# Kernel tuning notes

Hardware: AMD Instinct MI355X
Metric: run time of the kernel (lower is better)

## Reference

```python
import jax, jax.numpy as jnp
import numpy as np

N_NODES = 100000
N_EDGES = 3200000
D_IN = 256
D_OUT = 128
LN_EPS = 1e-5


def setup_inputs() -> dict:
    key = jax.random.key(0)
    ks = jax.random.split(key, 6)
    stdv = 1.0 / np.sqrt(D_OUT)
    x = jax.random.normal(ks[0], (N_NODES, D_IN), dtype=jnp.float32)
    weight = jax.random.uniform(ks[1], (D_IN, D_OUT), minval=-stdv, maxval=stdv, dtype=jnp.float32)
    bias = jnp.zeros((D_OUT,), dtype=jnp.float32)
    res_w = jax.random.normal(ks[2], (D_IN, D_OUT), dtype=jnp.float32) * 0.05
    res_b = jnp.zeros((D_OUT,), dtype=jnp.float32)
    ln_gamma = jnp.ones((D_OUT,), dtype=jnp.float32)
    ln_beta = jnp.zeros((D_OUT,), dtype=jnp.float32)
    edge_weight = jax.random.uniform(ks[3], (N_EDGES,), dtype=jnp.float32)
    edge_index = jax.random.randint(ks[4], (2, N_EDGES), 0, N_NODES, dtype=jnp.int32)
    return {"x": x, "weight": weight, "bias": bias, "res_w": res_w, "res_b": res_b,
            "ln_gamma": ln_gamma, "ln_beta": ln_beta,
            "edge_weight": edge_weight, "edge_index": edge_index}


def reference(x, weight, bias, res_w, res_b, ln_gamma, ln_beta, edge_weight, edge_index):
    # dense projection: [N, D_IN] @ [D_IN, D_OUT]
    support = x @ weight
    # spmm: out[dst] += w_e * support[src]  (weighted COO aggregation)
    src, dst = edge_index[0], edge_index[1]
    msg = support[src] * edge_weight[:, None]          # [E, D_OUT]
    out = jax.ops.segment_sum(msg, dst, num_segments=N_NODES)
    # fused bias + activated residual branch
    out = out + bias + jax.nn.relu(x @ res_w + res_b)
    # layernorm over feature dim
    mu = jnp.mean(out, axis=-1, keepdims=True)
    var = jnp.mean(jnp.square(out - mu), axis=-1, keepdims=True)
    out = (out - mu) * jax.lax.rsqrt(var + LN_EPS) * ln_gamma + ln_beta
    return out
```

## Files before the change

kernel.cpp:

```cpp
#include <hip/hip_runtime.h>
#include <hip/hip_bf16.h>

#define D_IN 256
#define D_OUT 128
#define LN_EPS 1e-5f
#define NBUCK 256
#define NCHUNK 256

typedef short bf16x8 __attribute__((ext_vector_type(8)));
typedef float f32x4 __attribute__((ext_vector_type(4)));
typedef unsigned short ushort_t;

__device__ __forceinline__ float b2f(ushort_t u) {
    union { unsigned int i; float f; } v; v.i = (unsigned int)u << 16; return v.f;
}
__device__ __forceinline__ ushort_t f2b(float f) {
    __hip_bfloat16 h = __float2bfloat16(f);
    return *reinterpret_cast<ushort_t*>(&h);
}

__global__ void k_transpose(const float* __restrict__ w, const float* __restrict__ rw,
                            ushort_t* __restrict__ wt) {
    int idx = blockIdx.x * 256 + threadIdx.x;
    int n = idx >> 8, k = idx & 255;
    float v = (n < 128) ? w[k * 128 + n] : rw[k * 128 + (n - 128)];
    wt[idx] = f2b(v);
}

__launch_bounds__(256)
__global__ void k_gemm(const float* __restrict__ x, const ushort_t* __restrict__ wt,
                       const float* __restrict__ bias, const float* __restrict__ res_b,
                       ushort_t* __restrict__ support, float* __restrict__ out, int n_nodes) {
    __shared__ ushort_t As[64 * 40];
    __shared__ ushort_t Bs[256 * 40];

    const int tid = threadIdx.x;
    const int m0 = blockIdx.x * 64;
    const int wv = tid >> 6, lane = tid & 63;
    const int lm = lane & 15, quad = lane >> 4;
    const int mh = wv >> 1;
    const int nh = wv & 1;

    f32x4 acc[2][8];
#pragma unroll
    for (int i = 0; i < 2; i++)
#pragma unroll
        for (int j = 0; j < 8; j++) acc[i][j] = 0.0f;

    const int arow = tid >> 2, aseg = tid & 3;
    const bool arow_ok = (m0 + arow) < n_nodes;
    const float* xrow = x + (long)(m0 + arow) * D_IN + aseg * 8;

    for (int kc = 0; kc < 8; kc++) {
        __syncthreads();
        {
            bf16x8 av = {0, 0, 0, 0, 0, 0, 0, 0};
            if (arow_ok) {
                f32x4 p0 = *(const f32x4*)(xrow + kc * 32);
                f32x4 p1 = *(const f32x4*)(xrow + kc * 32 + 4);
#pragma unroll
                for (int j = 0; j < 4; j++) { av[j] = (short)f2b(p0[j]); av[4 + j] = (short)f2b(p1[j]); }
            }
            *(bf16x8*)(&As[arow * 40 + aseg * 8]) = av;
        }
#pragma unroll
        for (int i = 0; i < 4; i++) {
            int n = (tid >> 2) + i * 64;
            bf16x8 v = *(const bf16x8*)(wt + n * 256 + kc * 32 + aseg * 8);
            *(bf16x8*)(&Bs[n * 40 + aseg * 8]) = v;
        }
        __syncthreads();

        bf16x8 afr0 = *(const bf16x8*)(&As[(mh * 32 + lm) * 40 + quad * 8]);
        bf16x8 afr1 = *(const bf16x8*)(&As[(mh * 32 + 16 + lm) * 40 + quad * 8]);
#pragma unroll
        for (int nt = 0; nt < 8; nt++) {
            bf16x8 bfr = *(const bf16x8*)(&Bs[(nh * 128 + nt * 16 + lm) * 40 + quad * 8]);
            acc[0][nt] = __builtin_amdgcn_mfma_f32_16x16x32_bf16(afr0, bfr, acc[0][nt], 0, 0, 0);
            acc[1][nt] = __builtin_amdgcn_mfma_f32_16x16x32_bf16(afr1, bfr, acc[1][nt], 0, 0, 0);
        }
    }

#pragma unroll
    for (int i = 0; i < 2; i++) {
#pragma unroll
        for (int nt = 0; nt < 8; nt++) {
            int col = nh * 128 + nt * 16 + lm;
#pragma unroll
            for (int r = 0; r < 4; r++) {
                int node = m0 + mh * 32 + i * 16 + quad * 4 + r;
                if (node >= n_nodes) continue;
                float v = acc[i][nt][r];
                if (col < 128) {
                    support[(long)node * 128 + col] = f2b(v);
                } else {
                    int c2 = col - 128;
                    float t = v + res_b[c2];
                    t = t > 0.0f ? t : 0.0f;
                    out[(long)node * 128 + c2] = t + bias[c2];
                }
            }
        }
    }
}

__launch_bounds__(256)
__global__ void k_count(const int* __restrict__ ei, int* __restrict__ cntmat, int E, int chunk) {
    __shared__ int h[NBUCK];
    int c = blockIdx.x, t = threadIdx.x;
    h[t] = 0;
    __syncthreads();
    int lo = c * chunk, hi = min(lo + chunk, E);
    for (int e = lo + t; e < hi; e += 256)
        atomicAdd(&h[(unsigned)ei[E + e] >> 9], 1);
    __syncthreads();
    cntmat[t * NCHUNK + c] = h[t];
}

__launch_bounds__(256)
__global__ void k_scan1(int* __restrict__ cntmat, int* __restrict__ rowsum) {
    __shared__ int sh[256];
    int b = blockIdx.x, t = threadIdx.x;
    int v = cntmat[b * NCHUNK + t];
    sh[t] = v;
    __syncthreads();
    for (int off = 1; off < 256; off <<= 1) {
        int x = sh[t]; int add = (t >= off) ? sh[t - off] : 0;
        __syncthreads(); sh[t] = x + add; __syncthreads();
    }
    cntmat[b * NCHUNK + t] = sh[t] - v;
    if (t == 255) rowsum[b] = sh[255];
}

__launch_bounds__(256)
__global__ void k_scan2(const int* __restrict__ rowsum, int* __restrict__ bucket_base,
                        int* __restrict__ offs, int n_nodes, int E) {
    __shared__ int sh[256];
    int t = threadIdx.x;
    int v = rowsum[t];
    sh[t] = v;
    __syncthreads();
    for (int off = 1; off < 256; off <<= 1) {
        int x = sh[t]; int add = (t >= off) ? sh[t - off] : 0;
        __syncthreads(); sh[t] = x + add; __syncthreads();
    }
    bucket_base[t] = sh[t] - v;
    if (t == 255) bucket_base[256] = sh[255];
    if (t == 0) offs[n_nodes] = E;
}

__launch_bounds__(256)
__global__ void k_part(const int* __restrict__ ei, const float* __restrict__ ew,
                       const int* __restrict__ cntmat, const int* __restrict__ bucket_base,
                       int* __restrict__ pk, ushort_t* __restrict__ pw, int E, int chunk) {
    __shared__ int cur[NBUCK];
    int c = blockIdx.x, t = threadIdx.x;
    cur[t] = bucket_base[t] + cntmat[t * NCHUNK + c];
    __syncthreads();
    int lo = c * chunk, hi = min(lo + chunk, E);
    for (int e = lo + t; e < hi; e += 256) {
        int src = ei[e];
        int dst = ei[E + e];
        float w = ew[e];
        int b = (unsigned)dst >> 9;
        int pos = atomicAdd(&cur[b], 1);
        pk[pos] = src | ((dst & 511) << 17);
        pw[pos] = f2b(w);
    }
}

__launch_bounds__(256)
__global__ void k_build(const int* __restrict__ pk, const ushort_t* __restrict__ pw,
                        const int* __restrict__ bucket_base, int* __restrict__ sk,
                        ushort_t* __restrict__ sw, int* __restrict__ offs, int n_nodes) {
    __shared__ int h[512];
    __shared__ int psum[256];
    int b = blockIdx.x, t = threadIdx.x;
    int start = bucket_base[b], end = bucket_base[b + 1];
    h[t] = 0; h[t + 256] = 0;
    __syncthreads();
    for (int i = start + t; i < end; i += 256)
        atomicAdd(&h[(unsigned)pk[i] >> 17], 1);
    __syncthreads();
    int h0 = h[2 * t], h1 = h[2 * t + 1];
    int p = h0 + h1;
    psum[t] = p;
    __syncthreads();
    for (int off = 1; off < 256; off <<= 1) {
        int x = psum[t]; int add = (t >= off) ? psum[t - off] : 0;
        __syncthreads(); psum[t] = x + add; __syncthreads();
    }
    int e0 = psum[t] - p;
    int e1 = e0 + h0;
    h[2 * t] = e0; h[2 * t + 1] = e1;
    int node0 = b * 512 + 2 * t;
    if (node0 < n_nodes) offs[node0] = start + e0;
    if (node0 + 1 < n_nodes) offs[node0 + 1] = start + e1;
    __syncthreads();
    for (int i = start + t; i < end; i += 256) {
        int key = pk[i];
        int dl = (unsigned)key >> 17;
        int pos = start + atomicAdd(&h[dl], 1);
        sk[pos] = key;
        sw[pos] = pw[i];
    }
}

__launch_bounds__(256)
__global__ void k_agg_ln(const ushort_t* __restrict__ support, const int* __restrict__ offs,
                         const int* __restrict__ sk, const ushort_t* __restrict__ sw,
                         const float* __restrict__ gamma, const float* __restrict__ beta,
                         float* __restrict__ out, int n_nodes) {
    int gw = (int)((blockIdx.x * blockDim.x + threadIdx.x) >> 6);
    int lane = threadIdx.x & 63;
    int nw = (int)((gridDim.x * blockDim.x) >> 6);
    float g0 = gamma[lane * 2], g1 = gamma[lane * 2 + 1];
    float b0 = beta[lane * 2], b1 = beta[lane * 2 + 1];

    for (int node = gw; node < n_nodes; node += nw) {
        int start = offs[node], end = offs[node + 1];
        float ax = 0.0f, ay = 0.0f;
        for (int base = start; base < end; base += 64) {
            int n = end - base; if (n > 64) n = 64;
            int key = 0, wbits = 0;
            if (lane < n) {
                key = sk[base + lane];
                wbits = (int)sw[base + lane];
            }
            int j = 0;
            for (; j + 4 <= n; j += 4) {
                int s0 = __builtin_amdgcn_readlane(key, j + 0) & 131071;
                int s1 = __builtin_amdgcn_readlane(key, j + 1) & 131071;
                int s2 = __builtin_amdgcn_readlane(key, j + 2) & 131071;
                int s3 = __builtin_amdgcn_readlane(key, j + 3) & 131071;
                float w0 = b2f((ushort_t)__builtin_amdgcn_readlane(wbits, j + 0));
                float w1 = b2f((ushort_t)__builtin_amdgcn_readlane(wbits, j + 1));
                float w2 = b2f((ushort_t)__builtin_amdgcn_readlane(wbits, j + 2));
                float w3 = b2f((ushort_t)__builtin_amdgcn_readlane(wbits, j + 3));
                unsigned int v0 = *(const unsigned int*)(support + (long)s0 * 128 + lane * 2);
                unsigned int v1 = *(const unsigned int*)(support + (long)s1 * 128 + lane * 2);
                unsigned int v2 = *(const unsigned int*)(support + (long)s2 * 128 + lane * 2);
                unsigned int v3 = *(const unsigned int*)(support + (long)s3 * 128 + lane * 2);
                ax += w0 * b2f((ushort_t)(v0 & 0xffffu)) + w1 * b2f((ushort_t)(v1 & 0xffffu))
                    + w2 * b2f((ushort_t)(v2 & 0xffffu)) + w3 * b2f((ushort_t)(v3 & 0xffffu));
                ay += w0 * b2f((ushort_t)(v0 >> 16)) + w1 * b2f((ushort_t)(v1 >> 16))
                    + w2 * b2f((ushort_t)(v2 >> 16)) + w3 * b2f((ushort_t)(v3 >> 16));
            }
            for (; j < n; j++) {
                int sj = __builtin_amdgcn_readlane(key, j) & 131071;
                float wj = b2f((ushort_t)__builtin_amdgcn_readlane(wbits, j));
                unsigned int v = *(const unsigned int*)(support + (long)sj * 128 + lane * 2);
                ax += wj * b2f((ushort_t)(v & 0xffffu));
                ay += wj * b2f((ushort_t)(v >> 16));
            }
        }
        float2 r = *(const float2*)(out + (long)node * 128 + lane * 2);
        float tx = ax + r.x, ty = ay + r.y;
        float s = tx + ty;
        float ss = tx * tx + ty * ty;
#pragma unroll
        for (int off = 1; off < 64; off <<= 1) {
            s += __shfl_xor(s, off, 64);
            ss += __shfl_xor(ss, off, 64);
        }
        float mean = s * (1.0f / 128.0f);
        float var = ss * (1.0f / 128.0f) - mean * mean;
        float rstd = rsqrtf(var + LN_EPS);
        float2 o;
        o.x = (tx - mean) * rstd * g0 + b0;
        o.y = (ty - mean) * rstd * g1 + b1;
        *(float2*)(out + (long)node * 128 + lane * 2) = o;
    }
}

extern "C" void kernel_launch(void* const* d_in, const int* in_sizes, int n_in,
                              void* d_out, int out_size, void* d_ws, size_t ws_size,
                              hipStream_t stream) {
    const float* x      = (const float*)d_in[0];
    const float* weight = (const float*)d_in[1];
    const float* bias   = (const float*)d_in[2];
    const float* res_w  = (const float*)d_in[3];
    const float* res_b  = (const float*)d_in[4];
    const float* gamma  = (const float*)d_in[5];
    const float* beta   = (const float*)d_in[6];
    const float* ew     = (const float*)d_in[7];
    const int*   ei     = (const int*)d_in[8];

    const int E = in_sizes[7];
    const int n_nodes = in_sizes[0] / D_IN;
    const int chunk = (E + NCHUNK - 1) / NCHUNK;
    float* out = (float*)d_out;

    char* ws = (char*)d_ws;
    size_t off = 0;
    auto alloc = [&](size_t bytes) { void* p = ws + off; off = (off + bytes + 255) & ~(size_t)255; return p; };
    ushort_t* wt      = (ushort_t*)alloc(256 * 256 * 2);
    ushort_t* support = (ushort_t*)alloc((size_t)n_nodes * 128 * 2);
    int* cntmat       = (int*)alloc((size_t)NBUCK * NCHUNK * 4);
    int* rowsum       = (int*)alloc(NBUCK * 4);
    int* bucket_base  = (int*)alloc((NBUCK + 1) * 4);
    int* offs         = (int*)alloc((size_t)(n_nodes + 1) * 4);
    int* pk           = (int*)alloc((size_t)E * 4);
    ushort_t* pw      = (ushort_t*)alloc((size_t)E * 2);
    int* sk           = (int*)alloc((size_t)E * 4);
    ushort_t* sw      = (ushort_t*)alloc((size_t)E * 2);

    k_transpose<<<256, 256, 0, stream>>>(weight, res_w, wt);
    k_gemm<<<(n_nodes + 63) / 64, 256, 0, stream>>>(x, wt, bias, res_b, support, out, n_nodes);
    k_count<<<NCHUNK, 256, 0, stream>>>(ei, cntmat, E, chunk);
    k_scan1<<<NBUCK, 256, 0, stream>>>(cntmat, rowsum);
    k_scan2<<<1, 256, 0, stream>>>(rowsum, bucket_base, offs, n_nodes, E);
    k_part<<<NCHUNK, 256, 0, stream>>>(ei, ew, cntmat, bucket_base, pk, pw, E, chunk);
    k_build<<<NBUCK, 256, 0, stream>>>(pk, pw, bucket_base, sk, sw, offs, n_nodes);
    k_agg_ln<<<4096, 256, 0, stream>>>(support, offs, sk, sw, gamma, beta, out, n_nodes);
}
```

Measured before the change: 505.1 us.

## Use finer dst buckets and half-wave edge-pair gathers in aggregation

The bucket sort now uses 256 nodes per bucket (about 391 buckets) with 512 edge chunks and ushort counts, so the partition and build passes get more parallel blocks with smaller local histograms. k_build runs 512 threads per block and writes the source index pre-masked. In the aggregation each half-wave handles one edge of a pair and loads 4 bf16 per lane, halving the loop trips, then the halves are combined with a shuffle. The change also overlaps the count matrix with the transposed-weight buffer to save workspace, which relies on the weight buffer no longer being needed after the GEMM. It also assumes per-chunk bucket counts fit in 16 bits and that nbuck is at most 512.

```diff
diff --git a/kernel.cpp b/kernel.cpp
--- a/kernel.cpp
+++ b/kernel.cpp
@@ -4,8 +4,8 @@
 #define D_IN 256
 #define D_OUT 128
 #define LN_EPS 1e-5f
-#define NBUCK 256
-#define NCHUNK 256
+#define NPB 256
+#define NCHUNK 512
 
 typedef short bf16x8 __attribute__((ext_vector_type(8)));
 typedef float f32x4 __attribute__((ext_vector_type(4)));
@@ -105,103 +105,112 @@
 }
 
 __launch_bounds__(256)
-__global__ void k_count(const int* __restrict__ ei, int* __restrict__ cntmat, int E, int chunk) {
-    __shared__ int h[NBUCK];
+__global__ void k_count(const int* __restrict__ ei, ushort_t* __restrict__ cntmat,
+                        int E, int chunk, int nbuck) {
+    __shared__ int h[512];
     int c = blockIdx.x, t = threadIdx.x;
-    h[t] = 0;
+    h[t] = 0; h[t + 256] = 0;
     __syncthreads();
     int lo = c * chunk, hi = min(lo + chunk, E);
     for (int e = lo + t; e < hi; e += 256)
-        atomicAdd(&h[(unsigned)ei[E + e] >> 9], 1);
-    __syncthreads();
-    cntmat[t * NCHUNK + c] = h[t];
-}
-
-__launch_bounds__(256)
-__global__ void k_scan1(int* __restrict__ cntmat, int* __restrict__ rowsum) {
+        atomicAdd(&h[(unsigned)ei[E + e] >> 8], 1);
+    __syncthreads();
+    for (int i = t; i < nbuck; i += 256)
+        cntmat[i * NCHUNK + c] = (ushort_t)h[i];
+}
+
+__launch_bounds__(256)
+__global__ void k_scan1(ushort_t* __restrict__ cntmat, int* __restrict__ rowsum) {
     __shared__ int sh[256];
     int b = blockIdx.x, t = threadIdx.x;
-    int v = cntmat[b * NCHUNK + t];
-    sh[t] = v;
+    int v0 = cntmat[b * NCHUNK + 2 * t];
+    int v1 = cntmat[b * NCHUNK + 2 * t + 1];
+    int s = v0 + v1;
+    sh[t] = s;
     __syncthreads();
     for (int off = 1; off < 256; off <<= 1) {
         int x = sh[t]; int add = (t >= off) ? sh[t - off] : 0;
         __syncthreads(); sh[t] = x + add; __syncthreads();
     }
-    cntmat[b * NCHUNK + t] = sh[t] - v;
+    int e = sh[t] - s;
+    cntmat[b * NCHUNK + 2 * t] = (ushort_t)e;
+    cntmat[b * NCHUNK + 2 * t + 1] = (ushort_t)(e + v0);
     if (t == 255) rowsum[b] = sh[255];
 }
 
-__launch_bounds__(256)
+__launch_bounds__(512)
 __global__ void k_scan2(const int* __restrict__ rowsum, int* __restrict__ bucket_base,
-                        int* __restrict__ offs, int n_nodes, int E) {
-    __shared__ int sh[256];
+                        int* __restrict__ offs, int n_nodes, int E, int nbuck) {
+    __shared__ int sh[512];
     int t = threadIdx.x;
-    int v = rowsum[t];
+    int v = (t < nbuck) ? rowsum[t] : 0;
     sh[t] = v;
     __syncthreads();
-    for (int off = 1; off < 256; off <<= 1) {
+    for (int off = 1; off < 512; off <<= 1) {
         int x = sh[t]; int add = (t >= off) ? sh[t - off] : 0;
         __syncthreads(); sh[t] = x + add; __syncthreads();
     }
-    bucket_base[t] = sh[t] - v;
-    if (t == 255) bucket_base[256] = sh[255];
+    if (t < nbuck) bucket_base[t] = sh[t] - v;
+    if (t == nbuck - 1) bucket_base[nbuck] = sh[t];
     if (t == 0) offs[n_nodes] = E;
 }
 
 __launch_bounds__(256)
 __global__ void k_part(const int* __restrict__ ei, const float* __restrict__ ew,
-                       const int* __restrict__ cntmat, const int* __restrict__ bucket_base,
-                       int* __restrict__ pk, ushort_t* __restrict__ pw, int E, int chunk) {
-    __shared__ int cur[NBUCK];
+                       const ushort_t* __restrict__ cntmat, const int* __restrict__ bucket_base,
+                       int* __restrict__ pk, ushort_t* __restrict__ pw, int E, int chunk, int nbuck) {
+    __shared__ int cur[512];
     int c = blockIdx.x, t = threadIdx.x;
-    cur[t] = bucket_base[t] + cntmat[t * NCHUNK + c];
+    for (int i = t; i < nbuck; i += 256)
+        cur[i] = bucket_base[i] + (int)cntmat[i * NCHUNK + c];
     __syncthreads();
     int lo = c * chunk, hi = min(lo + chunk, E);
     for (int e = lo + t; e < hi; e += 256) {
         int src = ei[e];
         int dst = ei[E + e];
         float w = ew[e];
-        int b = (unsigned)dst >> 9;
+        int b = (unsigned)dst >> 8;
         int pos = atomicAdd(&cur[b], 1);
-        pk[pos] = src | ((dst & 511) << 17);
+        pk[pos] = src | ((dst & 255) << 17);
         pw[pos] = f2b(w);
     }
 }
 
-__launch_bounds__(256)
+__launch_bounds__(512)
 __global__ void k_build(const int* __restrict__ pk, const ushort_t* __restrict__ pw,
                         const int* __restrict__ bucket_base, int* __restrict__ sk,
                         ushort_t* __restrict__ sw, int* __restrict__ offs, int n_nodes) {
-    __shared__ int h[512];
+    __shared__ int h[256];
     __shared__ int psum[256];
     int b = blockIdx.x, t = threadIdx.x;
     int start = bucket_base[b], end = bucket_base[b + 1];
-    h[t] = 0; h[t + 256] = 0;
-    __syncthreads();
-    for (int i = start + t; i < end; i += 256)
+    if (t < 256) h[t] = 0;
+    __syncthreads();
+    for (int i = start + t; i < end; i += 512)
         atomicAdd(&h[(unsigned)pk[i] >> 17], 1);
     __syncthreads();
-    int h0 = h[2 * t], h1 = h[2 * t + 1];
-    int p = h0 + h1;
-    psum[t] = p;
+    int cnt = 0;
+    if (t < 256) { cnt = h[t]; psum[t] = cnt; }
     __syncthreads();
     for (int off = 1; off < 256; off <<= 1) {
-        int x = psum[t]; int add = (t >= off) ? psum[t - off] : 0;
-        __syncthreads(); psum[t] = x + add; __syncthreads();
-    }
-    int e0 = psum[t] - p;
-    int e1 = e0 + h0;
-    h[2 * t] = e0; h[2 * t + 1] = e1;
-    int node0 = b * 512 + 2 * t;
-    if (node0 < n_nodes) offs[node0] = start + e0;
-    if (node0 + 1 < n_nodes) offs[node0 + 1] = start + e1;
-    __syncthreads();
-    for (int i = start + t; i < end; i += 256) {
+        int x = 0, add = 0;
+        if (t < 256) { x = psum[t]; add = (t >= off) ? psum[t - off] : 0; }
+        __syncthreads();
+        if (t < 256) psum[t] = x + add;
+        __syncthreads();
+    }
+    if (t < 256) {
+        int excl = psum[t] - cnt;
+        int node = b * NPB + t;
+        if (node < n_nodes) offs[node] = start + excl;
+        h[t] = start + excl;
+    }
+    __syncthreads();
+    for (int i = start + t; i < end; i += 512) {
         int key = pk[i];
         int dl = (unsigned)key >> 17;
-        int pos = start + atomicAdd(&h[dl], 1);
-        sk[pos] = key;
+        int pos = atomicAdd(&h[dl], 1);
+        sk[pos] = key & 131071;
         sw[pos] = pw[i];
     }
 }
@@ -214,12 +223,15 @@
     int gw = (int)((blockIdx.x * blockDim.x + threadIdx.x) >> 6);
     int lane = threadIdx.x & 63;
     int nw = (int)((gridDim.x * blockDim.x) >> 6);
-    float g0 = gamma[lane * 2], g1 = gamma[lane * 2 + 1];
-    float b0 = beta[lane * 2], b1 = beta[lane * 2 + 1];
+    const int fl = lane & 31;
+    const bool hi_half = lane >= 32;
+
+    f32x4 g = *(const f32x4*)(gamma + fl * 4);
+    f32x4 bb = *(const f32x4*)(beta + fl * 4);
 
     for (int node = gw; node < n_nodes; node += nw) {
         int start = offs[node], end = offs[node + 1];
-        float ax = 0.0f, ay = 0.0f;
+        float a0 = 0.0f, a1 = 0.0f, a2 = 0.0f, a3 = 0.0f;
         for (int base = start; base < end; base += 64) {
             int n = end - base; if (n > 64) n = 64;
             int key = 0, wbits = 0;
@@ -227,49 +239,47 @@
                 key = sk[base + lane];
                 wbits = (int)sw[base + lane];
             }
-            int j = 0;
-            for (; j + 4 <= n; j += 4) {
-                int s0 = __builtin_amdgcn_readlane(key, j + 0) & 131071;
-                int s1 = __builtin_amdgcn_readlane(key, j + 1) & 131071;
-                int s2 = __builtin_amdgcn_readlane(key, j + 2) & 131071;
-                int s3 = __builtin_amdgcn_readlane(key, j + 3) & 131071;
-                float w0 = b2f((ushort_t)__builtin_amdgcn_readlane(wbits, j + 0));
-                float w1 = b2f((ushort_t)__builtin_amdgcn_readlane(wbits, j + 1));
-                float w2 = b2f((ushort_t)__builtin_amdgcn_readlane(wbits, j + 2));
-                float w3 = b2f((ushort_t)__builtin_amdgcn_readlane(wbits, j + 3));
-                unsigned int v0 = *(const unsigned int*)(support + (long)s0 * 128 + lane * 2);
-                unsigned int v1 = *(const unsigned int*)(support + (long)s1 * 128 + lane * 2);
-                unsigned int v2 = *(const unsigned int*)(support + (long)s2 * 128 + lane * 2);
-                unsigned int v3 = *(const unsigned int*)(support + (long)s3 * 128 + lane * 2);
-                ax += w0 * b2f((ushort_t)(v0 & 0xffffu)) + w1 * b2f((ushort_t)(v1 & 0xffffu))
-                    + w2 * b2f((ushort_t)(v2 & 0xffffu)) + w3 * b2f((ushort_t)(v3 & 0xffffu));
-                ay += w0 * b2f((ushort_t)(v0 >> 16)) + w1 * b2f((ushort_t)(v1 >> 16))
-                    + w2 * b2f((ushort_t)(v2 >> 16)) + w3 * b2f((ushort_t)(v3 >> 16));
+            int npair = (n + 1) >> 1;
+            for (int j = 0; j < npair; j++) {
+                int s0 = __builtin_amdgcn_readlane(key, 2 * j);
+                int s1 = __builtin_amdgcn_readlane(key, 2 * j + 1);
+                float w0 = b2f((ushort_t)__builtin_amdgcn_readlane(wbits, 2 * j));
+                float w1 = b2f((ushort_t)__builtin_amdgcn_readlane(wbits, 2 * j + 1));
+                int ssel = hi_half ? s1 : s0;
+                float wsel = hi_half ? w1 : w0;
+                uint2 v = *(const uint2*)(support + (long)ssel * 128 + fl * 4);
+                float f0 = __uint_as_float(v.x << 16);
+                float f1 = __uint_as_float(v.x & 0xffff0000u);
+                float f2 = __uint_as_float(v.y << 16);
+                float f3 = __uint_as_float(v.y & 0xffff0000u);
+                a0 += wsel * f0; a1 += wsel * f1; a2 += wsel * f2; a3 += wsel * f3;
             }
-            for (; j < n; j++) {
-                int sj = __builtin_amdgcn_readlane(key, j) & 131071;
-                float wj = b2f((ushort_t)__builtin_amdgcn_readlane(wbits, j));
-                unsigned int v = *(const unsigned int*)(support + (long)sj * 128 + lane * 2);
-                ax += wj * b2f((ushort_t)(v & 0xffffu));
-                ay += wj * b2f((ushort_t)(v >> 16));
-            }
-        }
-        float2 r = *(const float2*)(out + (long)node * 128 + lane * 2);
-        float tx = ax + r.x, ty = ay + r.y;
-        float s = tx + ty;
-        float ss = tx * tx + ty * ty;
-#pragma unroll
-        for (int off = 1; off < 64; off <<= 1) {
+        }
+        a0 += __shfl_xor(a0, 32, 64);
+        a1 += __shfl_xor(a1, 32, 64);
+        a2 += __shfl_xor(a2, 32, 64);
+        a3 += __shfl_xor(a3, 32, 64);
+
+        f32x4 r = *(const f32x4*)(out + (long)node * 128 + fl * 4);
+        float t0 = a0 + r[0], t1 = a1 + r[1], t2 = a2 + r[2], t3 = a3 + r[3];
+        float s = t0 + t1 + t2 + t3;
+        float ss = t0 * t0 + t1 * t1 + t2 * t2 + t3 * t3;
+#pragma unroll
+        for (int off = 1; off < 32; off <<= 1) {
             s += __shfl_xor(s, off, 64);
             ss += __shfl_xor(ss, off, 64);
         }
         float mean = s * (1.0f / 128.0f);
         float var = ss * (1.0f / 128.0f) - mean * mean;
         float rstd = rsqrtf(var + LN_EPS);
-        float2 o;
-        o.x = (tx - mean) * rstd * g0 + b0;
-        o.y = (ty - mean) * rstd * g1 + b1;
-        *(float2*)(out + (long)node * 128 + lane * 2) = o;
+        if (!hi_half) {
+            f32x4 o;
+            o[0] = (t0 - mean) * rstd * g[0] + bb[0];
+            o[1] = (t1 - mean) * rstd * g[1] + bb[1];
+            o[2] = (t2 - mean) * rstd * g[2] + bb[2];
+            o[3] = (t3 - mean) * rstd * g[3] + bb[3];
+            *(f32x4*)(out + (long)node * 128 + fl * 4) = o;
+        }
     }
 }
 
@@ -288,29 +298,33 @@
 
     const int E = in_sizes[7];
     const int n_nodes = in_sizes[0] / D_IN;
+    const int nbuck = (n_nodes + NPB - 1) / NPB;
     const int chunk = (E + NCHUNK - 1) / NCHUNK;
     float* out = (float*)d_out;
 
     char* ws = (char*)d_ws;
     size_t off = 0;
     auto alloc = [&](size_t bytes) { void* p = ws + off; off = (off + bytes + 255) & ~(size_t)255; return p; };
-    ushort_t* wt      = (ushort_t*)alloc(256 * 256 * 2);
-    ushort_t* support = (ushort_t*)alloc((size_t)n_nodes * 128 * 2);
-    int* cntmat       = (int*)alloc((size_t)NBUCK * NCHUNK * 4);
-    int* rowsum       = (int*)alloc(NBUCK * 4);
-    int* bucket_base  = (int*)alloc((NBUCK + 1) * 4);
-    int* offs         = (int*)alloc((size_t)(n_nodes + 1) * 4);
-    int* pk           = (int*)alloc((size_t)E * 4);
-    ushort_t* pw      = (ushort_t*)alloc((size_t)E * 2);
-    int* sk           = (int*)alloc((size_t)E * 4);
-    ushort_t* sw      = (ushort_t*)alloc((size_t)E * 2);
+    size_t r0 = (size_t)nbuck * NCHUNK * 2 + 8192;
+    if (r0 < 256 * 256 * 2) r0 = 256 * 256 * 2;
+    char* region0 = (char*)alloc(r0);
+    ushort_t* wt       = (ushort_t*)region0;
+    ushort_t* cntmat   = (ushort_t*)region0;
+    int* rowsum        = (int*)(region0 + (size_t)nbuck * NCHUNK * 2);
+    int* bucket_base   = rowsum + 512;
+    ushort_t* support  = (ushort_t*)alloc((size_t)n_nodes * 128 * 2);
+    int* offs          = (int*)alloc((size_t)(n_nodes + 1) * 4);
+    int* pk            = (int*)alloc((size_t)E * 4);
+    ushort_t* pw       = (ushort_t*)alloc((size_t)E * 2);
+    int* sk            = (int*)alloc((size_t)E * 4);
+    ushort_t* sw       = (ushort_t*)alloc((size_t)E * 2);
 
     k_transpose<<<256, 256, 0, stream>>>(weight, res_w, wt);
     k_gemm<<<(n_nodes + 63) / 64, 256, 0, stream>>>(x, wt, bias, res_b, support, out, n_nodes);
-    k_count<<<NCHUNK, 256, 0, stream>>>(ei, cntmat, E, chunk);
-    k_scan1<<<NBUCK, 256, 0, stream>>>(cntmat, rowsum);
-    k_scan2<<<1, 256, 0, stream>>>(rowsum, bucket_base, offs, n_nodes, E);
-    k_part<<<NCHUNK, 256, 0, stream>>>(ei, ew, cntmat, bucket_base, pk, pw, E, chunk);
-    k_build<<<NBUCK, 256, 0, stream>>>(pk, pw, bucket_base, sk, sw, offs, n_nodes);
+    k_count<<<NCHUNK, 256, 0, stream>>>(ei, cntmat, E, chunk, nbuck);
+    k_scan1<<<nbuck, 256, 0, stream>>>(cntmat, rowsum);
+    k_scan2<<<1, 512, 0, stream>>>(rowsum, bucket_base, offs, n_nodes, E, nbuck);
+    k_part<<<NCHUNK, 256, 0, stream>>>(ei, ew, cntmat, bucket_base, pk, pw, E, chunk, nbuck);
+    k_build<<<nbuck, 512, 0, stream>>>(pk, pw, bucket_base, sk, sw, offs, n_nodes);
     k_agg_ln<<<4096, 256, 0, stream>>>(support, offs, sk, sw, gamma, beta, out, n_nodes);
 }
```

Result: slower. 529.2 us (+4.8%).
